# Kernel optimization log

Measured on AMD Instinct MI355X. Metric: run time of the kernel, lower is better.

## Reference

```python
import jax, jax.numpy as jnp
import numpy as np

NUM_EMB = 1024
EMB_DIM = 32


def setup_inputs() -> dict:
    key = jax.random.key(0)
    k1, k2 = jax.random.split(key)
    z = jax.random.normal(k1, (32, EMB_DIM, 64, 64), dtype=jnp.float32)
    # nn.Embedding weight init: uniform(-1/num_embeddings, 1/num_embeddings)
    emb_weight = jax.random.uniform(
        k2, (NUM_EMB, EMB_DIM), dtype=jnp.float32,
        minval=-1.0 / NUM_EMB, maxval=1.0 / NUM_EMB)
    return {"z": z, "emb_weight": emb_weight}


def reference(z, emb_weight):
    # z: [B, C, H, W] -> [B, H, W, C]
    z_p = jnp.transpose(z, (0, 2, 3, 1))
    B, H, W, C = z_p.shape
    z_flat = z_p.reshape(-1, C)  # [N, C]
    # squared distances via expansion: ||z||^2 + ||e||^2 - 2 z.e  -> [N, K]
    d = (jnp.sum(z_flat * z_flat, axis=1, keepdims=True)
         + jnp.sum(emb_weight * emb_weight, axis=1)
         - 2.0 * jnp.matmul(z_flat, emb_weight.T))
    idx = jnp.argmin(d, axis=1)  # [N]
    z_q = emb_weight[idx].reshape(B, H, W, C)
    # straight-through estimator (applied in BHWC, then back to BCHW)
    z_q = z_p + jax.lax.stop_gradient(z_q - z_p)
    z_q = jnp.transpose(z_q, (0, 3, 1, 2))  # [B, C, H, W]
    return z_q, idx
```

## Files before the change

### kernel.cpp

```cpp
#include <hip/hip_runtime.h>


#define NUM_EMB 1024
#define EMB_DIM 32
#define HW      4096
#define BATCH   32
#define N_TOT   (BATCH * HW)
#define NSPLIT  4
#define CODES_PER (NUM_EMB / NSPLIT)
#define MARGIN  1.0e-4f
#define CHUNK   256
#define ESTRIDE 36

#define OFF_BQ    0u
#define OFF_EH    4096u
#define OFF_EL    69632u
#define OFF_CTRS  135168u
#define OFF_LISTB 135184u
#define WS_NEED   659472u
#define WS_NEED_R7 (4096u + 4u * 131072u * 8u)

using bf16x8 = __attribute__((ext_vector_type(8))) short;
using bf16x4 = __attribute__((ext_vector_type(4))) short;
using f32x4  = __attribute__((ext_vector_type(4))) float;

#define REPEAT32(M) \
    M(0)  M(1)  M(2)  M(3)  M(4)  M(5)  M(6)  M(7)  \
    M(8)  M(9)  M(10) M(11) M(12) M(13) M(14) M(15) \
    M(16) M(17) M(18) M(19) M(20) M(21) M(22) M(23) \
    M(24) M(25) M(26) M(27) M(28) M(29) M(30) M(31)

__device__ __forceinline__ unsigned short bf16_rne(float x) {
    unsigned u = __float_as_uint(x);
    return (unsigned short)((u + 0x7FFFu + ((u >> 16) & 1u)) >> 16);
}

__device__ __forceinline__ float pairwise_sq32(const float* __restrict__ e) {
    float r0 = __fmul_rn(e[0], e[0]), r1 = __fmul_rn(e[1], e[1]);
    float r2 = __fmul_rn(e[2], e[2]), r3 = __fmul_rn(e[3], e[3]);
    float r4 = __fmul_rn(e[4], e[4]), r5 = __fmul_rn(e[5], e[5]);
    float r6 = __fmul_rn(e[6], e[6]), r7 = __fmul_rn(e[7], e[7]);
#pragma unroll
    for (int i = 8; i < 32; i += 8) {
        r0 = __fadd_rn(r0, __fmul_rn(e[i + 0], e[i + 0]));
        r1 = __fadd_rn(r1, __fmul_rn(e[i + 1], e[i + 1]));
        r2 = __fadd_rn(r2, __fmul_rn(e[i + 2], e[i + 2]));
        r3 = __fadd_rn(r3, __fmul_rn(e[i + 3], e[i + 3]));
        r4 = __fadd_rn(r4, __fmul_rn(e[i + 4], e[i + 4]));
        r5 = __fadd_rn(r5, __fmul_rn(e[i + 5], e[i + 5]));
        r6 = __fadd_rn(r6, __fmul_rn(e[i + 6], e[i + 6]));
        r7 = __fadd_rn(r7, __fmul_rn(e[i + 7], e[i + 7]));
    }
    return __fadd_rn(__fadd_rn(__fadd_rn(r0, r1), __fadd_rn(r2, r3)),
                     __fadd_rn(__fadd_rn(r4, r5), __fadd_rn(r6, r7)));
}

__device__ __forceinline__ void store_row16(unsigned short* dst,
                                            const unsigned short* v) {
    unsigned w[16];
#pragma unroll
    for (int i = 0; i < 16; ++i)
        w[i] = (unsigned)v[2 * i] | ((unsigned)v[2 * i + 1] << 16);
    uint4* d4 = (uint4*)dst;
    d4[0] = make_uint4(w[0], w[1], w[2], w[3]);
    d4[1] = make_uint4(w[4], w[5], w[6], w[7]);
    d4[2] = make_uint4(w[8], w[9], w[10], w[11]);
    d4[3] = make_uint4(w[12], w[13], w[14], w[15]);
}

__global__ __launch_bounds__(256) void vq_prep_e(
        const float* __restrict__ emb, float* __restrict__ bq,
        unsigned short* __restrict__ eh, unsigned short* __restrict__ el,
        int* __restrict__ ctrs) {
    const int g = blockIdx.x * 256 + threadIdx.x;
    if (g < 2) ctrs[g] = 0;
    if (g >= NUM_EMB) return;
    const float* e = emb + g * EMB_DIM;
    bq[g] = pairwise_sq32(e);
    unsigned short h[32], l[32];
#pragma unroll
    for (int c = 0; c < 32; ++c) {
        float v = -2.0f * e[c];
        unsigned short hb = bf16_rne(v);
        float hf = __uint_as_float((unsigned)hb << 16);
        l[c] = bf16_rne(v - hf);
        h[c] = hb;
    }
    store_row16(eh + (size_t)g * 32, h);
    store_row16(el + (size_t)g * 32, l);
}

__device__ __forceinline__ bf16x8 lds_read8(const short* p) {
    bf16x4 a = *(const bf16x4*)p;
    bf16x4 b = *(const bf16x4*)(p + 4);
    return __builtin_shufflevector(a, b, 0, 1, 2, 3, 4, 5, 6, 7);
}

#define LOADZ(c) float z##c = zp[(size_t)(c) * HW];
#define Z_SQ_A()                                                              \
    float r0 = __fmul_rn(z0, z0), r1 = __fmul_rn(z1, z1);                     \
    float r2 = __fmul_rn(z2, z2), r3 = __fmul_rn(z3, z3);                     \
    float r4 = __fmul_rn(z4, z4), r5 = __fmul_rn(z5, z5);                     \
    float r6 = __fmul_rn(z6, z6), r7 = __fmul_rn(z7, z7);                     \
    r0 = __fadd_rn(r0, __fmul_rn(z8,  z8));  r0 = __fadd_rn(r0, __fmul_rn(z16, z16)); \
    r0 = __fadd_rn(r0, __fmul_rn(z24, z24));                                  \
    r1 = __fadd_rn(r1, __fmul_rn(z9,  z9));  r1 = __fadd_rn(r1, __fmul_rn(z17, z17)); \
    r1 = __fadd_rn(r1, __fmul_rn(z25, z25));                                  \
    r2 = __fadd_rn(r2, __fmul_rn(z10, z10)); r2 = __fadd_rn(r2, __fmul_rn(z18, z18)); \
    r2 = __fadd_rn(r2, __fmul_rn(z26, z26));                                  \
    r3 = __fadd_rn(r3, __fmul_rn(z11, z11)); r3 = __fadd_rn(r3, __fmul_rn(z19, z19)); \
    r3 = __fadd_rn(r3, __fmul_rn(z27, z27));                                  \
    r4 = __fadd_rn(r4, __fmul_rn(z12, z12)); r4 = __fadd_rn(r4, __fmul_rn(z20, z20)); \
    r4 = __fadd_rn(r4, __fmul_rn(z28, z28));                                  \
    r5 = __fadd_rn(r5, __fmul_rn(z13, z13)); r5 = __fadd_rn(r5, __fmul_rn(z21, z21)); \
    r5 = __fadd_rn(r5, __fmul_rn(z29, z29));                                  \
    r6 = __fadd_rn(r6, __fmul_rn(z14, z14)); r6 = __fadd_rn(r6, __fmul_rn(z22, z22)); \
    r6 = __fadd_rn(r6, __fmul_rn(z30, z30));                                  \
    r7 = __fadd_rn(r7, __fmul_rn(z15, z15)); r7 = __fadd_rn(r7, __fmul_rn(z23, z23)); \
    r7 = __fadd_rn(r7, __fmul_rn(z31, z31));                                  \
    const float a = __fadd_rn(                                                \
        __fadd_rn(__fadd_rn(r0, r1), __fadd_rn(r2, r3)),                      \
        __fadd_rn(__fadd_rn(r4, r5), __fadd_rn(r6, r7)));

#define FMA1(k) m = __fmaf_rn(z##k, e[(k)], m);
#define EXACT_KEY(jv)                                                         \
    {                                                                         \
        const float* e = emb + (size_t)(jv) * EMB_DIM;                        \
        float m = 0.0f;                                                       \
        REPEAT32(FMA1)                                                        \
        float d = __fsub_rn(__fadd_rn(a, bq[(jv)]), __fmul_rn(2.0f, m));      \
        unsigned u = __float_as_uint(d);                                      \
        u = (u & 0x80000000u) ? ~u : (u | 0x80000000u);                       \
        unsigned long long kk =                                               \
            ((unsigned long long)u << 32) | (unsigned)(jv);                   \
        if (kk < bestk) bestk = kk;                                           \
    }

__global__ __launch_bounds__(256, 4) void vq_filter(
        const float* __restrict__ z, const float* __restrict__ emb,
        const unsigned short* __restrict__ eh,
        const unsigned short* __restrict__ el,
        const float* __restrict__ bq, int* __restrict__ ctrs,
        int* __restrict__ listB, float* __restrict__ out_zq,
        float* __restrict__ out_idx) {
    __shared__ __align__(16) char smem[37888];
    short* seh = (short*)smem;
    short* sel = (short*)(smem + 18432);
    float* sbq = (float*)(smem + 36864);
    float* sz    = (float*)smem;
    int*   scand = (int*)(smem + 16896);
    int*   sdest = (int*)(smem + 18944);
    int*   sidx  = (int*)(smem + 19456);
    __shared__ int swt[2];
    __shared__ int sbase1;

    const int tid  = threadIdx.x;
    const int lane = tid & 63;
    const int wv   = tid >> 6;
    const int cloc = lane & 15, quad = lane >> 4;
    const int qbase = blockIdx.x * 128 + wv * 32;

    float  zf[2][8];
    bf16x8 azh[2], azl[2];
#pragma unroll
    for (int t = 0; t < 2; ++t) {
        const int q  = qbase + t * 16 + cloc;
        const int b  = q >> 12;
        const int hw = q & 4095;
        const float* zb = z + ((size_t)b * EMB_DIM + quad * 8) * HW + hw;
#pragma unroll
        for (int k = 0; k < 8; ++k) {
            float v = zb[(size_t)k * HW];
            zf[t][k] = v;
            unsigned short hb = bf16_rne(v);
            float hf = __uint_as_float((unsigned)hb << 16);
            azh[t][k] = (short)hb;
            azl[t][k] = (short)bf16_rne(v - hf);
        }
    }

    float m1[2][4], m2[2][4];
    int   i1[2][4];
#pragma unroll
    for (int t = 0; t < 2; ++t)
#pragma unroll
        for (int r = 0; r < 4; ++r) {
            m1[t][r] = 3.4e38f; m2[t][r] = 3.4e38f; i1[t][r] = 0;
        }

    for (int ch = 0; ch < 4; ++ch) {
        if (ch) __syncthreads();
#pragma unroll
        for (int i = 0; i < 8; ++i) {
            const int chunk = i * 256 + tid;
            const int r = chunk >> 3, c = chunk & 7;
            *(uint2*)&seh[r * ESTRIDE + c * 4] =
                *(const uint2*)(eh + (size_t)(ch * CHUNK + r) * 32 + c * 4);
            *(uint2*)&sel[r * ESTRIDE + c * 4] =
                *(const uint2*)(el + (size_t)(ch * CHUNK + r) * 32 + c * 4);
        }
        sbq[tid] = bq[ch * CHUNK + tid];
        __syncthreads();

        for (int jt = 0; jt < 16; ++jt) {
            const int row = jt * 16 + cloc;
            bf16x8 efh = lds_read8(&seh[row * ESTRIDE + quad * 8]);
            bf16x8 efl = lds_read8(&sel[row * ESTRIDE + quad * 8]);
            const float bqv = sbq[row];
            const int jts = ch * 16 + jt;
#pragma unroll
            for (int t = 0; t < 2; ++t) {
                f32x4 acc = {bqv, bqv, bqv, bqv};
                acc = __builtin_amdgcn_mfma_f32_16x16x32_bf16(azl[t], efh, acc, 0, 0, 0);
                acc = __builtin_amdgcn_mfma_f32_16x16x32_bf16(azh[t], efl, acc, 0, 0, 0);
                acc = __builtin_amdgcn_mfma_f32_16x16x32_bf16(azh[t], efh, acc, 0, 0, 0);
#pragma unroll
                for (int r = 0; r < 4; ++r) {
                    const float tt = acc[r];
                    const bool l1 = tt < m1[t][r];
                    m2[t][r] = __builtin_amdgcn_fmed3f(tt, m1[t][r], m2[t][r]);
                    m1[t][r] = fminf(m1[t][r], tt);
                    i1[t][r] = l1 ? jts : i1[t][r];
                }
            }
        }
    }
    __syncthreads();

#pragma unroll
    for (int t = 0; t < 2; ++t) {
        const int ql = wv * 32 + t * 16 + cloc;
#pragma unroll
        for (int k = 0; k < 8; ++k) sz[ql * 33 + quad * 8 + k] = zf[t][k];
    }

    float g[2][4];
#pragma unroll
    for (int t = 0; t < 2; ++t)
#pragma unroll
        for (int r = 0; r < 4; ++r) g[t][r] = m1[t][r];
#pragma unroll
    for (int off = 1; off < 16; off <<= 1)
#pragma unroll
        for (int t = 0; t < 2; ++t)
#pragma unroll
            for (int r = 0; r < 4; ++r)
                g[t][r] = fminf(g[t][r], __shfl_xor(g[t][r], off, 64));

#pragma unroll
    for (int t = 0; t < 2; ++t)
#pragma unroll
        for (int r = 0; r < 4; ++r) {
            const float thr = g[t][r] + MARGIN;
            const int   ql  = wv * 32 + t * 16 + quad * 4 + r;
            const bool  f1  = m1[t][r] <= thr;
            const bool  f2  = m2[t][r] <= thr;
            const unsigned long long b1 = __ballot(f1);
            const unsigned long long b2 = __ballot(f2);
            const unsigned mk1 = (unsigned)(b1 >> (quad * 16)) & 0xFFFFu;
            const unsigned mk2 = (unsigned)(b2 >> (quad * 16)) & 0xFFFFu;
            const int pc  = __popc(mk1);
            const int ldr = __ffs(mk1) - 1;
            if (mk2 | (unsigned)(pc > 4)) {
                if (cloc == ldr) sdest[ql] = 5;
            } else {
                if (f1)
                    scand[(ql << 2) + __popc(mk1 & ((1u << cloc) - 1u))] =
                        i1[t][r] * 16 + cloc;
                if (cloc == ldr) sdest[ql] = pc;
            }
        }
    __syncthreads();

    int d = 0, pre = 0;
    if (tid < 128) {
        d = sdest[tid];
        const unsigned long long mB = __ballot(d == 5);
        pre = (int)__popcll(mB & ((1ull << lane) - 1ull));
        if (lane == 0) swt[tid >> 6] = (int)__popcll(mB);
    }
    __syncthreads();
    if (tid == 0) {
        const int tB = swt[0] + swt[1];
        sbase1 = tB ? atomicAdd(&ctrs[1], tB) : 0;
    }
    __syncthreads();
    if (tid < 128) {
        if (d == 5) {
            listB[sbase1 + ((tid >> 6) ? swt[0] : 0) + pre] =
                blockIdx.x * 128 + tid;
        } else if (d == 1) {
            sidx[tid] = scand[tid << 2];
        } else {
            const float* szp = &sz[tid * 33];
#define LOADZ2(c) const float z##c = szp[(c)];
            REPEAT32(LOADZ2)
#undef LOADZ2
            Z_SQ_A()
            unsigned long long bestk = ~0ull;
            for (int k = 0; k < d; ++k) {
                const int jv = scand[(tid << 2) + k];
                EXACT_KEY(jv)
            }
            sidx[tid] = (int)(unsigned)(bestk & 0xffffffffu);
        }
    }
    __syncthreads();

    if (tid < 128 && d != 5) {
        const int n    = blockIdx.x * 128 + tid;
        const int bidx = sidx[tid];
        out_idx[n] = (float)bidx;
        const int b  = n >> 12;
        const int hw = n & 4095;
        const float4* er = (const float4*)(emb + (size_t)bidx * EMB_DIM);
        float* op = out_zq + (size_t)b * EMB_DIM * HW + hw;
#pragma unroll
        for (int c4 = 0; c4 < 8; ++c4) {
            float4 v = er[c4];
            op[(size_t)(c4 * 4 + 0) * HW] = v.x;
            op[(size_t)(c4 * 4 + 1) * HW] = v.y;
            op[(size_t)(c4 * 4 + 2) * HW] = v.z;
            op[(size_t)(c4 * 4 + 3) * HW] = v.w;
        }
    }
}

__global__ __launch_bounds__(256) void vq_fixup(
        const float* __restrict__ z, const float* __restrict__ emb,
        const float* __restrict__ bq, const int* __restrict__ ctrs,
        const int* __restrict__ listB, float* __restrict__ out_zq,
        float* __restrict__ out_idx) {
    __shared__ unsigned long long bs[256];
    const int tid = threadIdx.x;
    const int total = ctrs[1];

    for (int it = blockIdx.x; it < total; it += gridDim.x) {
        const int n  = listB[it];
        const int b  = n >> 12;
        const int hw = n & 4095;
        const float* zp = z + (size_t)b * EMB_DIM * HW + hw;
        REPEAT32(LOADZ)
        Z_SQ_A()
        unsigned long long bestk = ~0ull;
#pragma unroll
        for (int k = 0; k < 4; ++k) { const int jv = tid * 4 + k; EXACT_KEY(jv) }
        bs[tid] = bestk;
        __syncthreads();
        for (int off = 128; off > 0; off >>= 1) {
            if (tid < off && bs[tid + off] < bs[tid]) bs[tid] = bs[tid + off];
            __syncthreads();
        }
        const int bidx = (int)(unsigned)(bs[0] & 0xffffffffu);
        if (tid == 0) out_idx[n] = (float)bidx;
        if (tid < EMB_DIM)
            out_zq[(size_t)b * EMB_DIM * HW + (size_t)tid * HW + hw] =
                emb[(size_t)bidx * EMB_DIM + tid];
        __syncthreads();
    }
}

#define SCAN_GROUP4(j)                                                        \
    {                                                                         \
        const float* e = emb + (size_t)(j) * EMB_DIM;                         \
        const float bq0 = bq[(j) + 0], bq1 = bq[(j) + 1];                     \
        const float bq2 = bq[(j) + 2], bq3 = bq[(j) + 3];                     \
        float m0 = 0.0f, m1 = 0.0f, m2 = 0.0f, m3 = 0.0f;                     \
        REPEAT32(FMA_K)                                                       \
        float d0 = __fsub_rn(__fadd_rn(a, bq0), __fmul_rn(2.0f, m0));         \
        float d1 = __fsub_rn(__fadd_rn(a, bq1), __fmul_rn(2.0f, m1));         \
        float d2 = __fsub_rn(__fadd_rn(a, bq2), __fmul_rn(2.0f, m2));         \
        float d3 = __fsub_rn(__fadd_rn(a, bq3), __fmul_rn(2.0f, m3));         \
        if (d0 < best) { best = d0; bidx = (j) + 0; }                         \
        if (d1 < best) { best = d1; bidx = (j) + 1; }                         \
        if (d2 < best) { best = d2; bidx = (j) + 2; }                         \
        if (d3 < best) { best = d3; bidx = (j) + 3; }                         \
    }
#define FMA_K(k) \
        m0 = __fmaf_rn(z##k, e[0 * EMB_DIM + (k)], m0); \
        m1 = __fmaf_rn(z##k, e[1 * EMB_DIM + (k)], m1); \
        m2 = __fmaf_rn(z##k, e[2 * EMB_DIM + (k)], m2); \
        m3 = __fmaf_rn(z##k, e[3 * EMB_DIM + (k)], m3);

__global__ __launch_bounds__(256) void vq_sqnorm_kernel(
        const float* __restrict__ emb, float* __restrict__ bq) {
    int j = blockIdx.x * 256 + threadIdx.x;
    if (j < NUM_EMB) bq[j] = pairwise_sq32(emb + j * EMB_DIM);
}

__global__ __launch_bounds__(128, 4) void vq_partial_kernel(
        const float* __restrict__ z, const float* __restrict__ emb,
        const float* __restrict__ bq, unsigned long long* __restrict__ pk) {
    const int n  = blockIdx.x * 128 + threadIdx.x;
    const int b  = n >> 12;
    const int hw = n & 4095;
    const float* zp = z + (size_t)b * EMB_DIM * HW + hw;
    REPEAT32(LOADZ)
    Z_SQ_A()
    const int j0 = blockIdx.y * CODES_PER;
    float best = 3.4e38f;
    int   bidx = j0;
    for (int j = j0; j < j0 + CODES_PER; j += 4) SCAN_GROUP4(j)
    pk[(size_t)blockIdx.y * N_TOT + n] =
        ((unsigned long long)__float_as_uint(best) << 32) | (unsigned)bidx;
}

__global__ __launch_bounds__(256, 2) void vq_main_kernel(
        const float* __restrict__ z, const float* __restrict__ emb,
        const float* __restrict__ bq, float* __restrict__ out_zq,
        float* __restrict__ out_idx) {
    const int n  = blockIdx.x * 256 + threadIdx.x;
    const int b  = n >> 12;
    const int hw = n & 4095;
    const float* zp = z + (size_t)b * EMB_DIM * HW + hw;
    REPEAT32(LOADZ)
    Z_SQ_A()
    float best = 3.4e38f;
    int   bidx = 0;
    for (int j = 0; j < NUM_EMB; j += 4) SCAN_GROUP4(j)
    out_idx[n] = (float)bidx;
    const float* eb = emb + (size_t)bidx * EMB_DIM;
    float* op = out_zq + (size_t)b * EMB_DIM * HW + hw;
#pragma unroll
    for (int cc = 0; cc < EMB_DIM; ++cc) op[(size_t)cc * HW] = eb[cc];
}

__global__ __launch_bounds__(256) void vq_combine_kernel(
        const float* __restrict__ emb,
        const unsigned long long* __restrict__ pk,
        float* __restrict__ out_zq, float* __restrict__ out_idx) {
    const int n = blockIdx.x * 256 + threadIdx.x;
    unsigned long long m = pk[n];
#pragma unroll
    for (int y = 1; y < NSPLIT; ++y) {
        unsigned long long v = pk[(size_t)y * N_TOT + n];
        if (v < m) m = v;
    }
    const int bidx = (int)(unsigned)(m & 0xffffffffu);
    out_idx[n] = (float)bidx;
    const int b  = n >> 12;
    const int hw = n & 4095;
    const float* eb = emb + (size_t)bidx * EMB_DIM;
    float* op = out_zq + (size_t)b * EMB_DIM * HW + hw;
#pragma unroll
    for (int cc = 0; cc < EMB_DIM; ++cc) op[(size_t)cc * HW] = eb[cc];
}

extern "C" void kernel_launch(void* const* d_in, const int* in_sizes, int n_in,
                              void* d_out, int out_size, void* d_ws,
                              size_t ws_size, hipStream_t stream) {
    const float* z   = (const float*)d_in[0];
    const float* emb = (const float*)d_in[1];
    char* ws = (char*)d_ws;
    float* out0 = (float*)d_out;
    float* out1 = out0 + (size_t)BATCH * EMB_DIM * HW;

    if (ws_size >= WS_NEED) {
        float*          bq    = (float*)(ws + OFF_BQ);
        unsigned short* eh    = (unsigned short*)(ws + OFF_EH);
        unsigned short* el    = (unsigned short*)(ws + OFF_EL);
        int*            ctrs  = (int*)(ws + OFF_CTRS);
        int*            listB = (int*)(ws + OFF_LISTB);

        vq_prep_e<<<4, 256, 0, stream>>>(emb, bq, eh, el, ctrs);
        vq_filter<<<N_TOT / 128, 256, 0, stream>>>(z, emb, eh, el, bq, ctrs,
                                                   listB, out0, out1);
        vq_fixup<<<1024, 256, 0, stream>>>(z, emb, bq, ctrs, listB,
                                           out0, out1);
    } else if (ws_size >= WS_NEED_R7) {
        float* bq = (float*)ws;
        unsigned long long* pk = (unsigned long long*)(ws + 4096);
        vq_sqnorm_kernel<<<NUM_EMB / 256, 256, 0, stream>>>(emb, bq);
        vq_partial_kernel<<<dim3(N_TOT / 128, NSPLIT), 128, 0, stream>>>(
            z, emb, bq, pk);
        vq_combine_kernel<<<N_TOT / 256, 256, 0, stream>>>(emb, pk, out0, out1);
    } else {
        float* bq = (float*)ws;
        vq_sqnorm_kernel<<<NUM_EMB / 256, 256, 0, stream>>>(emb, bq);
        vq_main_kernel<<<N_TOT / 256, 256, 0, stream>>>(z, emb, bq, out0, out1);
    }
}
```

Measured before the change: 130.9 us.

## Replace split-bf16 triple MFMA filter with single fp16 MFMA

The filter pass approximated distances with three bf16 MFMAs over a hi/lo split of z and the codebook. It now uses one fp16 MFMA on fp16-rounded values, drops the low-part codebook buffer and its shared-memory staging, and raises the occupancy hint to 8 blocks per CU. The goal is to cut MFMA work, LDS traffic and shared memory per block. The trade-off is a coarser first-pass distance, so the fixed MARGIN may let more points through to the exact fixup pass, or miss the true argmin if the fp16 error exceeds the margin.

```diff
diff --git a/kernel.cpp b/kernel.cpp
--- a/kernel.cpp
+++ b/kernel.cpp
@@ -10,30 +10,22 @@
 #define CODES_PER (NUM_EMB / NSPLIT)
 #define MARGIN  1.0e-4f
 #define CHUNK   256
-#define ESTRIDE 36
 
 #define OFF_BQ    0u
 #define OFF_EH    4096u
-#define OFF_EL    69632u
 #define OFF_CTRS  135168u
 #define OFF_LISTB 135184u
 #define WS_NEED   659472u
 #define WS_NEED_R7 (4096u + 4u * 131072u * 8u)
 
-using bf16x8 = __attribute__((ext_vector_type(8))) short;
-using bf16x4 = __attribute__((ext_vector_type(4))) short;
-using f32x4  = __attribute__((ext_vector_type(4))) float;
+using f16x8 = __attribute__((ext_vector_type(8))) _Float16;
+using f32x4 = __attribute__((ext_vector_type(4))) float;
 
 #define REPEAT32(M) \
     M(0)  M(1)  M(2)  M(3)  M(4)  M(5)  M(6)  M(7)  \
     M(8)  M(9)  M(10) M(11) M(12) M(13) M(14) M(15) \
     M(16) M(17) M(18) M(19) M(20) M(21) M(22) M(23) \
     M(24) M(25) M(26) M(27) M(28) M(29) M(30) M(31)
-
-__device__ __forceinline__ unsigned short bf16_rne(float x) {
-    unsigned u = __float_as_uint(x);
-    return (unsigned short)((u + 0x7FFFu + ((u >> 16) & 1u)) >> 16);
-}
 
 __device__ __forceinline__ float pairwise_sq32(const float* __restrict__ e) {
     float r0 = __fmul_rn(e[0], e[0]), r1 = __fmul_rn(e[1], e[1]);
@@ -70,30 +62,19 @@
 
 __global__ __launch_bounds__(256) void vq_prep_e(
         const float* __restrict__ emb, float* __restrict__ bq,
-        unsigned short* __restrict__ eh, unsigned short* __restrict__ el,
-        int* __restrict__ ctrs) {
+        unsigned short* __restrict__ eh, int* __restrict__ ctrs) {
     const int g = blockIdx.x * 256 + threadIdx.x;
     if (g < 2) ctrs[g] = 0;
     if (g >= NUM_EMB) return;
     const float* e = emb + g * EMB_DIM;
     bq[g] = pairwise_sq32(e);
-    unsigned short h[32], l[32];
+    unsigned short h[32];
 #pragma unroll
     for (int c = 0; c < 32; ++c) {
-        float v = -2.0f * e[c];
-        unsigned short hb = bf16_rne(v);
-        float hf = __uint_as_float((unsigned)hb << 16);
-        l[c] = bf16_rne(v - hf);
-        h[c] = hb;
+        _Float16 hv = (_Float16)(-2.0f * e[c]);
+        h[c] = __builtin_bit_cast(unsigned short, hv);
     }
     store_row16(eh + (size_t)g * 32, h);
-    store_row16(el + (size_t)g * 32, l);
-}
-
-__device__ __forceinline__ bf16x8 lds_read8(const short* p) {
-    bf16x4 a = *(const bf16x4*)p;
-    bf16x4 b = *(const bf16x4*)(p + 4);
-    return __builtin_shufflevector(a, b, 0, 1, 2, 3, 4, 5, 6, 7);
 }
 
 #define LOADZ(c) float z##c = zp[(size_t)(c) * HW];
@@ -136,17 +117,15 @@
         if (kk < bestk) bestk = kk;                                           \
     }
 
-__global__ __launch_bounds__(256, 4) void vq_filter(
+__global__ __launch_bounds__(256, 8) void vq_filter(
         const float* __restrict__ z, const float* __restrict__ emb,
         const unsigned short* __restrict__ eh,
-        const unsigned short* __restrict__ el,
         const float* __restrict__ bq, int* __restrict__ ctrs,
         int* __restrict__ listB, float* __restrict__ out_zq,
         float* __restrict__ out_idx) {
-    __shared__ __align__(16) char smem[37888];
-    short* seh = (short*)smem;
-    short* sel = (short*)(smem + 18432);
-    float* sbq = (float*)(smem + 36864);
+    __shared__ __align__(16) char smem[19968];
+    _Float16* seh = (_Float16*)smem;
+    float*    sbq = (float*)(smem + 16384);
     float* sz    = (float*)smem;
     int*   scand = (int*)(smem + 16896);
     int*   sdest = (int*)(smem + 18944);
@@ -160,8 +139,8 @@
     const int cloc = lane & 15, quad = lane >> 4;
     const int qbase = blockIdx.x * 128 + wv * 32;
 
-    float  zf[2][8];
-    bf16x8 azh[2], azl[2];
+    float zf[2][8];
+    f16x8 az[2];
 #pragma unroll
     for (int t = 0; t < 2; ++t) {
         const int q  = qbase + t * 16 + cloc;
@@ -172,10 +151,7 @@
         for (int k = 0; k < 8; ++k) {
             float v = zb[(size_t)k * HW];
             zf[t][k] = v;
-            unsigned short hb = bf16_rne(v);
-            float hf = __uint_as_float((unsigned)hb << 16);
-            azh[t][k] = (short)hb;
-            azl[t][k] = (short)bf16_rne(v - hf);
+            az[t][k] = (_Float16)v;
         }
     }
 
@@ -190,30 +166,24 @@
 
     for (int ch = 0; ch < 4; ++ch) {
         if (ch) __syncthreads();
-#pragma unroll
-        for (int i = 0; i < 8; ++i) {
-            const int chunk = i * 256 + tid;
-            const int r = chunk >> 3, c = chunk & 7;
-            *(uint2*)&seh[r * ESTRIDE + c * 4] =
-                *(const uint2*)(eh + (size_t)(ch * CHUNK + r) * 32 + c * 4);
-            *(uint2*)&sel[r * ESTRIDE + c * 4] =
-                *(const uint2*)(el + (size_t)(ch * CHUNK + r) * 32 + c * 4);
-        }
-        sbq[tid] = bq[ch * CHUNK + tid];
+        {
+            const uint4* src = (const uint4*)(eh + (size_t)ch * CHUNK * 32);
+            uint4* dst = (uint4*)seh;
+#pragma unroll
+            for (int i = 0; i < 4; ++i) dst[i * 256 + tid] = src[i * 256 + tid];
+            sbq[tid] = bq[ch * CHUNK + tid];
+        }
         __syncthreads();
 
         for (int jt = 0; jt < 16; ++jt) {
             const int row = jt * 16 + cloc;
-            bf16x8 efh = lds_read8(&seh[row * ESTRIDE + quad * 8]);
-            bf16x8 efl = lds_read8(&sel[row * ESTRIDE + quad * 8]);
+            f16x8 ef = *(const f16x8*)(seh + row * 32 + quad * 8);
             const float bqv = sbq[row];
             const int jts = ch * 16 + jt;
 #pragma unroll
             for (int t = 0; t < 2; ++t) {
                 f32x4 acc = {bqv, bqv, bqv, bqv};
-                acc = __builtin_amdgcn_mfma_f32_16x16x32_bf16(azl[t], efh, acc, 0, 0, 0);
-                acc = __builtin_amdgcn_mfma_f32_16x16x32_bf16(azh[t], efl, acc, 0, 0, 0);
-                acc = __builtin_amdgcn_mfma_f32_16x16x32_bf16(azh[t], efh, acc, 0, 0, 0);
+                acc = __builtin_amdgcn_mfma_f32_16x16x32_f16(az[t], ef, acc, 0, 0, 0);
 #pragma unroll
                 for (int r = 0; r < 4; ++r) {
                     const float tt = acc[r];
@@ -458,12 +428,11 @@
     if (ws_size >= WS_NEED) {
         float*          bq    = (float*)(ws + OFF_BQ);
         unsigned short* eh    = (unsigned short*)(ws + OFF_EH);
-        unsigned short* el    = (unsigned short*)(ws + OFF_EL);
         int*            ctrs  = (int*)(ws + OFF_CTRS);
         int*            listB = (int*)(ws + OFF_LISTB);
 
-        vq_prep_e<<<4, 256, 0, stream>>>(emb, bq, eh, el, ctrs);
-        vq_filter<<<N_TOT / 128, 256, 0, stream>>>(z, emb, eh, el, bq, ctrs,
+        vq_prep_e<<<4, 256, 0, stream>>>(emb, bq, eh, ctrs);
+        vq_filter<<<N_TOT / 128, 256, 0, stream>>>(z, emb, eh, bq, ctrs,
                                                    listB, out0, out1);
         vq_fixup<<<1024, 256, 0, stream>>>(z, emb, bq, ctrs, listB,
                                            out0, out1);
```

Result: slower. 147.0 us (+12.3%).
